# Optimization experiments

Hardware: AMD Instinct MI355X
Metric: run time of the kernel (lower is better)

Reference implementation:

```python
import jax, jax.numpy as jnp
import numpy as np

KERNEL_SIZE = 13
SIGMA_MIN, SIGMA_MAX = 0.4, 10.0
BETA, THRESHOLD = 0.95, 1.0


@jax.custom_vjp
def spike(x):
    # Heaviside forward, snntorch ATan surrogate backward (alpha=2)
    return (x > 0).astype(x.dtype)

def _spike_fwd(x):
    return spike(x), x

def _spike_bwd(x, g):
    return (g / (1.0 + (jnp.pi * x) ** 2),)

spike.defvjp(_spike_fwd, _spike_bwd)


def setup_inputs() -> dict:
    key = jax.random.key(0)
    k1, k2 = jax.random.split(key)
    B, C, T = 32, 224, 2048
    inp = jax.random.normal(k1, (B, 1, C, T), dtype=jnp.float32)
    linear_w = jax.random.normal(k2, (1, C), dtype=jnp.float32) * (1.0 / np.sqrt(C))
    return {"inp": inp, "linear_w": linear_w}


def _forward(inp, linear_w):
    x = inp[:, 0]  # [B, C, T]
    B, C, T = x.shape
    sigma_mean = 0.5 * (SIGMA_MIN + SIGMA_MAX)
    # adaptive sigma per (batch, time): Linear over channel axis, no bias
    w = sigma_mean + jnp.einsum('bct,c->bt', x, linear_w[0]) * (SIGMA_MAX - SIGMA_MIN)
    w = jnp.clip(w, SIGMA_MIN, SIGMA_MAX)  # [B, T]

    half = KERNEL_SIZE // 2
    r = jnp.linspace(-half, half, KERNEL_SIZE)
    r_all = jnp.linspace(-half * 10, half * 10, KERNEL_SIZE * 10)
    sig = w[..., None]  # [B, T, 1]
    kern = jnp.exp(-0.5 * (r / sig) ** 2)                       # [B, T, K]
    norm = jnp.exp(-0.5 * (r_all / sig) ** 2).sum(-1, keepdims=True)
    kern = kern / norm                                          # normalized over fine grid

    # adaptive gaussian smoothing along the CHANNEL axis (per timestep kernel)
    xt = jnp.transpose(x, (0, 2, 1))                            # [B, T, C]
    padded = jnp.pad(xt, ((0, 0), (0, 0), (half, half)))        # zero pad channels
    x_mean = sum(padded[:, :, k:k + C] * kern[:, :, k:k + 1]
                 for k in range(KERNEL_SIZE))                   # [B, T, C]
    x_mean = jnp.transpose(x_mean, (0, 2, 1))                   # [B, C, T]

    I = x - jax.nn.relu(x - x_mean)                             # soft min(x, x_mean)

    # Leaky-integrate-and-fire over time (snntorch Leaky, reset-by-subtract)
    def step(mem, I_t):
        reset = jax.lax.stop_gradient((mem > THRESHOLD).astype(I_t.dtype))
        mem = BETA * mem + I_t - reset * THRESHOLD
        spk = spike(mem - THRESHOLD)
        return mem, spk

    I_seq = jnp.transpose(I, (2, 0, 1))                         # [T, B, C]
    _, spk = jax.lax.scan(step, jnp.zeros((B, C), I.dtype), I_seq)
    spk = jnp.transpose(spk, (1, 2, 0))                         # [B, C, T]
    return spk[:, None]                                         # [B, 1, C, T]


def reference(inp, linear_w):
    return _forward(inp, linear_w)
```

## Files before the change

### kernel.cpp

```cpp
#include <hip/hip_runtime.h>
#include <math.h>

#define BB 32
#define CCH 224
#define TTT 2048
#define TPB 64
#define NT  (TTT/TPB)
#define CG  28
#define NCG (CCH/CG)
#define ROWS 40
#define XROW 68
#define IROW 29

__device__ __forceinline__ void bar_lds() {
    asm volatile("s_waitcnt lgkmcnt(0)" ::: "memory");
    __builtin_amdgcn_s_barrier();
    asm volatile("" ::: "memory");
}

__global__ __launch_bounds__(256) void kw(
    const float* __restrict__ x, const float* __restrict__ lw,
    double* __restrict__ kernG)
{
    __shared__ double sp[4][64];
    const int b  = blockIdx.y;
    const int tl = threadIdx.x & 63;
    const int q  = threadIdx.x >> 6;
    const int t  = blockIdx.x * 64 + tl;

    const float* xb  = x + (((size_t)(b * CCH + 56 * q)) << 11) + t;
    const float* lwq = lw + 56 * q;

    double p = 0.0;
    #pragma unroll 8
    for (int i = 0; i < 56; ++i)
        p += (double)xb[(size_t)i << 11] * (double)lwq[i];
    sp[q][tl] = p;
    __syncthreads();

    if (threadIdx.x < 64) {
        double acc = (sp[0][tl] + sp[1][tl]) + (sp[2][tl] + sp[3][tl]);

        double w = 5.2 + acc * 9.6;
        w = fmin(fmax(w, 0.4), 10.0);
        double iw2 = 1.0 / (w * w);

        const double s = 120.0 / 129.0;
        double G  = exp(-0.125 * s * s * iw2);
        double G2 = G * G, G4 = G2 * G2, G8 = G4 * G4;
        double term = G, cmul = G8, norm = G;
        for (int u = 1; u <= 64; ++u) { term *= cmul; cmul *= G8; norm += term; }
        norm *= 2.0;

        double P = exp(-0.5 * iw2), P2 = P * P;
        double a = 1.0, bm = P, inv = 1.0 / norm;
        double* kr = kernG + (size_t)(b * TTT + t) * 7;
        kr[0] = inv;
        #pragma unroll
        for (int d = 1; d <= 6; ++d) {
            a *= bm; bm *= P2;
            kr[d] = a * inv;
        }
    }
}

__global__ __launch_bounds__(320) void kf(
    const float* __restrict__ x, const double* __restrict__ kernG,
    float* __restrict__ out)
{
    __shared__ __align__(16) float xs[2][ROWS][XROW];
    __shared__ double kd[2][TPB][7];
    __shared__ double Is[2][TPB][IROW];
    __shared__ unsigned long long bitsb[2][CG];

    const int b   = blockIdx.y;
    const int cgi = blockIdx.x;
    const int c0  = cgi * CG;
    const int tid = threadIdx.x;
    const int ctid = tid - 64;

    const float*  xbase = x + (((size_t)(b * CCH)) << 11);
    const double* kbase = kernG + (size_t)(b * TTT) * 7;
    float* obase = out + (((size_t)(b * CCH + c0)) << 11);

    double mem = 0.0;
    bool   r   = false;

    float4 rv[3]; double kv[7];

    if (tid >= 64) {
        #pragma unroll
        for (int i2 = 0; i2 < 3; ++i2) {
            int e = ctid + i2 * 256;
            if (e < ROWS * 16) {
                int rr = e >> 4, q = e & 15;
                int cr = c0 - 6 + rr;
                float4 v = make_float4(0.f, 0.f, 0.f, 0.f);
                if (cr >= 0 && cr < CCH)
                    v = *(const float4*)(xbase + ((size_t)cr << 11) + 4 * q);
                *(float4*)&xs[0][rr][4 * q] = v;
            }
        }
        if (ctid < TPB) {
            const double* kp = kbase + (size_t)ctid * 7;
            #pragma unroll
            for (int i2 = 0; i2 < 7; ++i2) kd[0][ctid][i2] = kp[i2];
        }
        {
            const int gt0 = TPB;
            #pragma unroll
            for (int i2 = 0; i2 < 3; ++i2) {
                int e = ctid + i2 * 256;
                if (e < ROWS * 16) {
                    int rr = e >> 4, q = e & 15;
                    int cr = c0 - 6 + rr;
                    rv[i2] = make_float4(0.f, 0.f, 0.f, 0.f);
                    if (cr >= 0 && cr < CCH)
                        rv[i2] = *(const float4*)(xbase + ((size_t)cr << 11) + gt0 + 4 * q);
                }
            }
            if (ctid < TPB) {
                const double* kp = kbase + (size_t)(gt0 + ctid) * 7;
                #pragma unroll
                for (int i2 = 0; i2 < 7; ++i2) kv[i2] = kp[i2];
            }
        }
    }
    bar_lds();

    for (int k = 0; k <= NT + 1; ++k) {
        if (tid >= 64) {
            const int buf = k & 1, nbuf = (k + 1) & 1;
            if (k + 1 <= NT - 1) {
                #pragma unroll
                for (int i2 = 0; i2 < 3; ++i2) {
                    int e = ctid + i2 * 256;
                    if (e < ROWS * 16) {
                        int rr = e >> 4, q = e & 15;
                        *(float4*)&xs[nbuf][rr][4 * q] = rv[i2];
                    }
                }
                if (ctid < TPB) {
                    #pragma unroll
                    for (int i2 = 0; i2 < 7; ++i2) kd[nbuf][ctid][i2] = kv[i2];
                }
            }
            if (k + 2 <= NT - 1) {
                const int gt0 = (k + 2) * TPB;
                #pragma unroll
                for (int i2 = 0; i2 < 3; ++i2) {
                    int e = ctid + i2 * 256;
                    if (e < ROWS * 16) {
                        int rr = e >> 4, q = e & 15;
                        int cr = c0 - 6 + rr;
                        rv[i2] = make_float4(0.f, 0.f, 0.f, 0.f);
                        if (cr >= 0 && cr < CCH)
                            rv[i2] = *(const float4*)(xbase + ((size_t)cr << 11) + gt0 + 4 * q);
                    }
                }
                if (ctid < TPB) {
                    const double* kp = kbase + (size_t)(gt0 + ctid) * 7;
                    #pragma unroll
                    for (int i2 = 0; i2 < 7; ++i2) kv[i2] = kp[i2];
                }
            }
            if (k >= 2) {
                const int j = k - 2, jb = j & 1;
                const int t0o = j * TPB;
                #pragma unroll
                for (int i2 = 0; i2 < 2; ++i2) {
                    int e = ctid + i2 * 256;
                    if (e < CG * 16) {
                        int c = e >> 4, q = e & 15;
                        unsigned long long bits = bitsb[jb][c] >> (4 * q);
                        float4 v;
                        v.x = (bits & 1ull) ? 1.0f : 0.0f;
                        v.y = (bits & 2ull) ? 1.0f : 0.0f;
                        v.z = (bits & 4ull) ? 1.0f : 0.0f;
                        v.w = (bits & 8ull) ? 1.0f : 0.0f;
                        *(float4*)(obase + ((size_t)c << 11) + t0o + 4 * q) = v;
                    }
                }
            }
            if (k <= NT - 1) {
                const int t  = ctid & 63;
                const int ch = ctid >> 6;
                const int cb = 7 * ch;
                double kk7[7];
                #pragma unroll
                for (int i2 = 0; i2 < 7; ++i2) kk7[i2] = kd[buf][t][i2];
                float xv[13];
                #pragma unroll
                for (int i2 = 0; i2 < 13; ++i2) xv[i2] = xs[buf][cb + i2][t];
                #pragma unroll
                for (int c = 0; c < 7; ++c) {
                    double acc = 0.0;
                    #pragma unroll
                    for (int kk2 = 0; kk2 < 13; ++kk2) {
                        int d = kk2 < 6 ? 6 - kk2 : kk2 - 6;
                        acc = fma((double)xv[(c + kk2) % 13], kk7[d], acc);
                    }
                    double xvv = (double)xv[(c + 6) % 13];
                    double dd  = xvv - acc;
                    Is[buf][t][cb + c] = xvv - (dd > 0.0 ? dd : 0.0);
                    if (c < 6) xv[c % 13] = xs[buf][cb + c + 13][t];
                }
            }
        } else {
            if (k >= 1 && k <= NT) {
                const int p = (k - 1) & 1;
                const int c = tid;
                __builtin_amdgcn_s_setprio(1);
                if (c < CG) {
                    unsigned long long bits = 0ull;
                    double va[8], vb[8];
                    #pragma unroll
                    for (int j2 = 0; j2 < 8; ++j2) va[j2] = Is[p][j2][c];
                    #pragma unroll
                    for (int g = 0; g < 64; g += 16) {
                        #pragma unroll
                        for (int j2 = 0; j2 < 8; ++j2) vb[j2] = Is[p][g + 8 + j2][c];
                        #pragma unroll
                        for (int j2 = 0; j2 < 8; ++j2) {
                            double a2 = va[j2];
                            double cm = a2 - 1.0;
                            double m1 = fma(0.95, mem, a2);
                            double m2 = fma(0.95, mem, cm);
                            mem = r ? m2 : m1;
                            r = mem > 1.0;
                            bits |= (unsigned long long)(r ? 1 : 0) << (g + j2);
                        }
                        if (g + 16 < 64) {
                            #pragma unroll
                            for (int j2 = 0; j2 < 8; ++j2) va[j2] = Is[p][g + 16 + j2][c];
                        }
                        #pragma unroll
                        for (int j2 = 0; j2 < 8; ++j2) {
                            double a2 = vb[j2];
                            double cm = a2 - 1.0;
                            double m1 = fma(0.95, mem, a2);
                            double m2 = fma(0.95, mem, cm);
                            mem = r ? m2 : m1;
                            r = mem > 1.0;
                            bits |= (unsigned long long)(r ? 1 : 0) << (g + 8 + j2);
                        }
                    }
                    bitsb[p][c] = bits;
                }
                __builtin_amdgcn_s_setprio(0);
            }
        }
        bar_lds();
    }
}

extern "C" void kernel_launch(void* const* d_in, const int* in_sizes, int n_in,
                              void* d_out, int out_size, void* d_ws, size_t ws_size,
                              hipStream_t stream)
{
    const float* x  = (const float*)d_in[0];
    const float* lw = (const float*)d_in[1];
    float* out = (float*)d_out;

    double* kernG = (double*)d_ws;

    kw<<<dim3(TTT / 64, BB), 256, 0, stream>>>(x, lw, kernG);
    kf<<<dim3(NCG, BB), 320, 0, stream>>>(x, kernG, out);
}
```

Measured before the change: 146.4 us.

## Widen compute threads to 448 and shorten LIF recurrence critical path

```diff
diff --git a/kernel.cpp b/kernel.cpp
--- a/kernel.cpp
+++ b/kernel.cpp
@@ -11,6 +11,8 @@
 #define ROWS 40
 #define XROW 68
 #define IROW 29
+#define CPW 4
+#define CTH 448
 
 __device__ __forceinline__ void bar_lds() {
     asm volatile("s_waitcnt lgkmcnt(0)" ::: "memory");
@@ -64,7 +66,7 @@
     }
 }
 
-__global__ __launch_bounds__(320) void kf(
+__global__ __launch_bounds__(512) void kf(
     const float* __restrict__ x, const double* __restrict__ kernG,
     float* __restrict__ out)
 {
@@ -86,12 +88,12 @@
     double mem = 0.0;
     bool   r   = false;
 
-    float4 rv[3]; double kv[7];
+    float4 rv[2]; double kv[7];
 
     if (tid >= 64) {
         #pragma unroll
-        for (int i2 = 0; i2 < 3; ++i2) {
-            int e = ctid + i2 * 256;
+        for (int i2 = 0; i2 < 2; ++i2) {
+            int e = ctid + i2 * CTH;
             if (e < ROWS * 16) {
                 int rr = e >> 4, q = e & 15;
                 int cr = c0 - 6 + rr;
@@ -109,8 +111,8 @@
         {
             const int gt0 = TPB;
             #pragma unroll
-            for (int i2 = 0; i2 < 3; ++i2) {
-                int e = ctid + i2 * 256;
+            for (int i2 = 0; i2 < 2; ++i2) {
+                int e = ctid + i2 * CTH;
                 if (e < ROWS * 16) {
                     int rr = e >> 4, q = e & 15;
                     int cr = c0 - 6 + rr;
@@ -133,8 +135,8 @@
             const int buf = k & 1, nbuf = (k + 1) & 1;
             if (k + 1 <= NT - 1) {
                 #pragma unroll
-                for (int i2 = 0; i2 < 3; ++i2) {
-                    int e = ctid + i2 * 256;
+                for (int i2 = 0; i2 < 2; ++i2) {
+                    int e = ctid + i2 * CTH;
                     if (e < ROWS * 16) {
                         int rr = e >> 4, q = e & 15;
                         *(float4*)&xs[nbuf][rr][4 * q] = rv[i2];
@@ -148,8 +150,8 @@
             if (k + 2 <= NT - 1) {
                 const int gt0 = (k + 2) * TPB;
                 #pragma unroll
-                for (int i2 = 0; i2 < 3; ++i2) {
-                    int e = ctid + i2 * 256;
+                for (int i2 = 0; i2 < 2; ++i2) {
+                    int e = ctid + i2 * CTH;
                     if (e < ROWS * 16) {
                         int rr = e >> 4, q = e & 15;
                         int cr = c0 - 6 + rr;
@@ -167,43 +169,37 @@
             if (k >= 2) {
                 const int j = k - 2, jb = j & 1;
                 const int t0o = j * TPB;
-                #pragma unroll
-                for (int i2 = 0; i2 < 2; ++i2) {
-                    int e = ctid + i2 * 256;
-                    if (e < CG * 16) {
-                        int c = e >> 4, q = e & 15;
-                        unsigned long long bits = bitsb[jb][c] >> (4 * q);
-                        float4 v;
-                        v.x = (bits & 1ull) ? 1.0f : 0.0f;
-                        v.y = (bits & 2ull) ? 1.0f : 0.0f;
-                        v.z = (bits & 4ull) ? 1.0f : 0.0f;
-                        v.w = (bits & 8ull) ? 1.0f : 0.0f;
-                        *(float4*)(obase + ((size_t)c << 11) + t0o + 4 * q) = v;
-                    }
-                }
+                int c = ctid >> 4, q = ctid & 15;
+                unsigned long long bits = bitsb[jb][c] >> (4 * q);
+                float4 v;
+                v.x = (bits & 1ull) ? 1.0f : 0.0f;
+                v.y = (bits & 2ull) ? 1.0f : 0.0f;
+                v.z = (bits & 4ull) ? 1.0f : 0.0f;
+                v.w = (bits & 8ull) ? 1.0f : 0.0f;
+                *(float4*)(obase + ((size_t)c << 11) + t0o + 4 * q) = v;
             }
             if (k <= NT - 1) {
                 const int t  = ctid & 63;
-                const int ch = ctid >> 6;
-                const int cb = 7 * ch;
+                const int g  = ctid >> 6;
+                const int cb = CPW * g;
                 double kk7[7];
                 #pragma unroll
                 for (int i2 = 0; i2 < 7; ++i2) kk7[i2] = kd[buf][t][i2];
-                float xv[13];
-                #pragma unroll
-                for (int i2 = 0; i2 < 13; ++i2) xv[i2] = xs[buf][cb + i2][t];
-                #pragma unroll
-                for (int c = 0; c < 7; ++c) {
+                double xv[13];
+                #pragma unroll
+                for (int i2 = 0; i2 < 13; ++i2) xv[i2] = (double)xs[buf][cb + i2][t];
+                #pragma unroll
+                for (int c = 0; c < CPW; ++c) {
                     double acc = 0.0;
                     #pragma unroll
                     for (int kk2 = 0; kk2 < 13; ++kk2) {
                         int d = kk2 < 6 ? 6 - kk2 : kk2 - 6;
-                        acc = fma((double)xv[(c + kk2) % 13], kk7[d], acc);
-                    }
-                    double xvv = (double)xv[(c + 6) % 13];
+                        acc = fma(xv[(c + kk2) % 13], kk7[d], acc);
+                    }
+                    double xvv = xv[(c + 6) % 13];
                     double dd  = xvv - acc;
                     Is[buf][t][cb + c] = xvv - (dd > 0.0 ? dd : 0.0);
-                    if (c < 6) xv[c % 13] = xs[buf][cb + c + 13][t];
+                    if (c < CPW - 1) xv[c % 13] = (double)xs[buf][cb + c + 13][t];
                 }
             }
         } else {
@@ -213,34 +209,34 @@
                 __builtin_amdgcn_s_setprio(1);
                 if (c < CG) {
                     unsigned long long bits = 0ull;
-                    double va[8], vb[8];
+                    double va[8], vb[8], ca[8], cb2[8];
                     #pragma unroll
                     for (int j2 = 0; j2 < 8; ++j2) va[j2] = Is[p][j2][c];
                     #pragma unroll
+                    for (int j2 = 0; j2 < 8; ++j2) ca[j2] = va[j2] - 1.0;
+                    #pragma unroll
                     for (int g = 0; g < 64; g += 16) {
                         #pragma unroll
                         for (int j2 = 0; j2 < 8; ++j2) vb[j2] = Is[p][g + 8 + j2][c];
                         #pragma unroll
+                        for (int j2 = 0; j2 < 8; ++j2) cb2[j2] = vb[j2] - 1.0;
+                        #pragma unroll
                         for (int j2 = 0; j2 < 8; ++j2) {
-                            double a2 = va[j2];
-                            double cm = a2 - 1.0;
-                            double m1 = fma(0.95, mem, a2);
-                            double m2 = fma(0.95, mem, cm);
-                            mem = r ? m2 : m1;
+                            double ax = r ? ca[j2] : va[j2];
+                            mem = fma(0.95, mem, ax);
                             r = mem > 1.0;
                             bits |= (unsigned long long)(r ? 1 : 0) << (g + j2);
                         }
                         if (g + 16 < 64) {
                             #pragma unroll
                             for (int j2 = 0; j2 < 8; ++j2) va[j2] = Is[p][g + 16 + j2][c];
+                            #pragma unroll
+                            for (int j2 = 0; j2 < 8; ++j2) ca[j2] = va[j2] - 1.0;
                         }
                         #pragma unroll
                         for (int j2 = 0; j2 < 8; ++j2) {
-                            double a2 = vb[j2];
-                            double cm = a2 - 1.0;
-                            double m1 = fma(0.95, mem, a2);
-                            double m2 = fma(0.95, mem, cm);
-                            mem = r ? m2 : m1;
+                            double ax = r ? cb2[j2] : vb[j2];
+                            mem = fma(0.95, mem, ax);
                             r = mem > 1.0;
                             bits |= (unsigned long long)(r ? 1 : 0) << (g + 8 + j2);
                         }
@@ -265,5 +261,5 @@
     double* kernG = (double*)d_ws;
 
     kw<<<dim3(TTT / 64, BB), 256, 0, stream>>>(x, lw, kernG);
-    kf<<<dim3(NCG, BB), 320, 0, stream>>>(x, kernG, out);
-}
+    kf<<<dim3(NCG, BB), 512, 0, stream>>>(x, kernG, out);
+}
```

Result: no change. 146.0 us (-0.3%).
